# Performance work log

Hardware: AMD Instinct MI355X
Metric: run time of the kernel (lower is better)

## Reference

```python
import jax, jax.numpy as jnp
import numpy as np

ML, KS, L = 3, 7, 7  # mL, kernelSize, L = 2*mL+1


def _conv(img, kern, pad, groups=1):
    # img: [N,C,H,W], kern: [O, C//groups, kh, kw]
    return jax.lax.conv_general_dilated(
        img, kern, (1, 1), [(pad, pad), (pad, pad)],
        dimension_numbers=("NCHW", "OIHW", "NCHW"),
        feature_group_count=groups)


def setup_inputs() -> dict:
    key = jax.random.key(0)
    ks = jax.random.split(key, 16)
    B, MU = 64, 256
    lin = lambda k, fi, fo: (jax.random.normal(k, (fi, fo), jnp.float32) / np.sqrt(fi)).astype(jnp.float32)
    return {
        "x": jax.random.normal(ks[0], (B, 1, MU, MU), jnp.float32),
        "f": jax.random.normal(ks[1], (B, 1, MU, MU), jnp.float32),
        "kernelA": jax.random.normal(ks[2], (B, 1, 3, 3), jnp.float32),
        "fc1_w1": lin(ks[3], 9, 200), "fc1_b1": jnp.zeros((200,), jnp.float32),
        "fc1_w2": lin(ks[4], 200, ML * KS * KS), "fc1_b2": jnp.zeros((ML * KS * KS,), jnp.float32),
        "fc2_w1": lin(ks[5], 9, 200), "fc2_b1": jnp.zeros((200,), jnp.float32),
        "fc2_w2": lin(ks[6], 200, ML * ML * KS * KS), "fc2_b2": jnp.zeros((ML * ML * KS * KS,), jnp.float32),
    }


def reference(x, f, kernelA, fc1_w1, fc1_b1, fc1_w2, fc1_b2, fc2_w1, fc2_b1, fc2_w2, fc2_b2):
    B, _, mu, _ = x.shape
    pad = KS // 2

    # residual r = f - A x   (per-sample 3x3 stencil conv, grouped)
    r = f - jax.vmap(lambda xi, ki: _conv(xi[None], ki[None], 1)[0])(x, kernelA)  # [B,1,mu,mu]

    # meta-MLPs produce per-sample dynamic conv kernels from the 3x3 stencil
    kA = kernelA.reshape(B, 9)
    h1 = jax.nn.relu(kA @ fc1_w1 + fc1_b1)
    w1 = (h1 @ fc1_w2 + fc1_b2).reshape(B, ML, 1, KS, KS)
    h2 = jax.nn.relu(kA @ fc2_w1 + fc2_b1)
    w2 = (h2 @ fc2_w2 + fc2_b2).reshape(B, ML, ML, KS, KS)

    # per-sample dynamic convs (batched via vmap)
    G1 = jax.vmap(lambda ri, wi: _conv(ri[None], wi, pad)[0])(r, w1)    # [B,mL,mu,mu]
    G2 = jax.vmap(lambda gi, wi: _conv(gi[None], wi, pad)[0])(G1, w2)   # [B,mL,mu,mu]
    G = jnp.concatenate([r, G1, G2], axis=1)                            # [B,L,mu,mu]

    # S = A G : apply per-sample stencil to each of the L channels (depthwise)
    S = jax.vmap(lambda gi, ki: _conv(gi[None], jnp.broadcast_to(ki[None], (L, 1, 3, 3)), 1, groups=L)[0])(G, kernelA)
    S = S.reshape(B, L, mu * mu)
    Gf = G.reshape(B, L, mu * mu)
    lr = r.reshape(B, mu * mu, 1)

    # normal equations: (S S^T) K = S r, tiny [L,L] solve per sample
    M = jnp.einsum("bln,bmn->blm", S, S)    # [B,L,L]
    b = jnp.matmul(S, lr)                   # [B,L,1]
    K = jnp.linalg.solve(M, b)              # [B,L,1]

    x_new = x + jnp.matmul(K.transpose(0, 2, 1), Gf).reshape(B, 1, mu, mu)
    return x_new
```

## Files before the change

kernel.cpp:

```cpp
#include <hip/hip_runtime.h>
#include <hip/hip_fp16.h>

#define MU 256
#define NPIX (MU*MU)
#define ML 3
#define KS 7
#define LCH 7
#define NENT 35
#define RBLK 128

typedef _Float16 half2r __attribute__((ext_vector_type(2)));

__device__ __forceinline__ float dot2f(half2r a, half2r b, float c) {
#if __has_builtin(__builtin_amdgcn_fdot2)
    return __builtin_amdgcn_fdot2(a, b, c, false);
#else
    return c + (float)a.x*(float)b.x + (float)a.y*(float)b.y;
#endif
}

__device__ __forceinline__ float4 load_h4(const __half* p) {
    __half2 a = *(const __half2*)p;
    __half2 b = *(const __half2*)(p + 2);
    float2 fa = __half22float2(a), fb = __half22float2(b);
    return make_float4(fa.x, fa.y, fb.x, fb.y);
}

__global__ void mlp_kernel(const float* __restrict__ kernelA,
                           const float* __restrict__ fc1_w1, const float* __restrict__ fc1_b1,
                           const float* __restrict__ fc1_w2, const float* __restrict__ fc1_b2,
                           const float* __restrict__ fc2_w1, const float* __restrict__ fc2_b1,
                           const float* __restrict__ fc2_w2, const float* __restrict__ fc2_b2,
                           half2r* __restrict__ w1p, half2r* __restrict__ w2p) {
    int b = blockIdx.x;
    int t = threadIdx.x;
    __shared__ float kA[9];
    __shared__ float h1[200], h2[200];
    __shared__ float w1s[147];
    __shared__ float w2s[441];
    if (t < 9) kA[t] = kernelA[b*9 + t];
    __syncthreads();
    if (t < 200) {
        float s1 = fc1_b1[t], s2 = fc2_b1[t];
        #pragma unroll
        for (int i = 0; i < 9; ++i) {
            s1 += kA[i] * fc1_w1[i*200 + t];
            s2 += kA[i] * fc2_w1[i*200 + t];
        }
        h1[t] = fmaxf(s1, 0.f);
        h2[t] = fmaxf(s2, 0.f);
    }
    __syncthreads();
    if (t < 147) {
        float s = fc1_b2[t];
        for (int i = 0; i < 200; ++i) s += h1[i] * fc1_w2[i*147 + t];
        w1s[t] = s;
    }
    for (int o = t; o < 441; o += 256) {
        float s = fc2_b2[o];
        for (int i = 0; i < 200; ++i) s += h2[i] * fc2_w2[i*441 + o];
        w2s[o] = s;
    }
    __syncthreads();
    for (int u = t; u < 168; u += 256) {
        int grp = u / 8, p = u % 8;
        int co = grp % 3, i = grp / 3;
        const float* w = &w1s[co*49 + i*7];
        float lo, hi;
        if (p < 4) { lo = (p == 0) ? 0.f : w[2*p - 1]; hi = w[2*p]; }
        else       { int q = p - 4; lo = w[2*q]; hi = (q == 3) ? 0.f : w[2*q + 1]; }
        half2r hp; hp.x = (_Float16)lo; hp.y = (_Float16)hi;
        w1p[(size_t)b*168 + u] = hp;
    }
    for (int u = t; u < 504; u += 256) {
        int grp = u / 8, p = u % 8;
        int co = grp % 3, i = (grp / 3) % 7, c = grp / 21;
        const float* w = &w2s[co*147 + c*49 + i*7];
        float lo, hi;
        if (p < 4) { lo = (p == 0) ? 0.f : w[2*p - 1]; hi = w[2*p]; }
        else       { int q = p - 4; lo = w[2*q]; hi = (q == 3) ? 0.f : w[2*q + 1]; }
        half2r hp; hp.x = (_Float16)lo; hp.y = (_Float16)hi;
        w2p[(size_t)b*504 + u] = hp;
    }
}

__global__ __launch_bounds__(256) void res_g1_kernel(
        const float* __restrict__ x, const float* __restrict__ f,
        const float* __restrict__ kA, const half2r* __restrict__ w1p,
        __half* __restrict__ r, __half* __restrict__ G1) {
    int b = blockIdx.z;
    __shared__ float xt[24][144];
    __shared__ _Float16 rt[22][136];
    int tx = threadIdx.x;
    int ty = threadIdx.y;
    int tid = ty*64 + tx;
    int x0 = blockIdx.x*128, y0 = blockIdx.y*16;
    const float* xb = x + (size_t)b*NPIX;
    const float* fb = f + (size_t)b*NPIX;
    const half2r* wp = w1p + (size_t)b*168;
    float k[9];
    #pragma unroll
    for (int i = 0; i < 9; ++i) k[i] = kA[b*9 + i];

    for (int u = tid; u < 24*36; u += 256) {
        int row = u / 36, q4 = u % 36;
        int yy = y0 + row - 4;
        int xx = x0 - 8 + q4*4;
        float4 vv = make_float4(0.f, 0.f, 0.f, 0.f);
        if (yy >= 0 && yy < MU && xx >= 0 && xx < MU)
            vv = *(const float4*)(xb + yy*MU + xx);
        *(float4*)&xt[row][q4*4] = vv;
    }
    __syncthreads();

    for (int u = tid; u < 22*34; u += 256) {
        int row = u / 34, c4 = u % 34;
        int Y = y0 - 3 + row;
        int X = x0 - 4 + 4*c4;
        bool inb = (Y >= 0 && Y < MU && X >= 0 && X < MU);
        float4 fv = make_float4(0.f, 0.f, 0.f, 0.f);
        if (inb) fv = *(const float4*)(fb + Y*MU + X);
        float fr[4] = {fv.x, fv.y, fv.z, fv.w};
        float rr[4];
        #pragma unroll
        for (int cc = 0; cc < 4; ++cc) {
            float s = 0.f;
            #pragma unroll
            for (int di = 0; di < 3; ++di)
                #pragma unroll
                for (int dj = 0; dj < 3; ++dj)
                    s += xt[row + di][4*c4 + 3 + cc + dj] * k[di*3 + dj];
            rr[cc] = inb ? (fr[cc] - s) : 0.f;
        }
        __half2 h01 = __float22half2_rn(make_float2(rr[0], rr[1]));
        __half2 h23 = __float22half2_rn(make_float2(rr[2], rr[3]));
        *(__half2*)&rt[row][4*c4]     = h01;
        *(__half2*)&rt[row][4*c4 + 2] = h23;
    }
    __syncthreads();

    float accA[3][4], accB[3][4];
    #pragma unroll
    for (int co = 0; co < 3; ++co)
        #pragma unroll
        for (int dy = 0; dy < 4; ++dy) { accA[co][dy] = 0.f; accB[co][dy] = 0.f; }

    int ry = ty*4;
    #pragma unroll
    for (int ir = 0; ir < 10; ++ir) {
        half2r P[5];
        #pragma unroll
        for (int q = 0; q < 5; ++q)
            P[q] = *(const half2r*)&rt[ry + ir][2*tx + 2*q];
        #pragma unroll
        for (int dy = 0; dy < 4; ++dy) {
            int i = ir - dy;
            if (i >= 0 && i <= 6) {
                #pragma unroll
                for (int co = 0; co < 3; ++co) {
                    const half2r* wv = wp + (i*3 + co)*8;
                    accA[co][dy] = dot2f(P[0], wv[0], accA[co][dy]);
                    accA[co][dy] = dot2f(P[1], wv[1], accA[co][dy]);
                    accA[co][dy] = dot2f(P[2], wv[2], accA[co][dy]);
                    accA[co][dy] = dot2f(P[3], wv[3], accA[co][dy]);
                    accB[co][dy] = dot2f(P[1], wv[4], accB[co][dy]);
                    accB[co][dy] = dot2f(P[2], wv[5], accB[co][dy]);
                    accB[co][dy] = dot2f(P[3], wv[6], accB[co][dy]);
                    accB[co][dy] = dot2f(P[4], wv[7], accB[co][dy]);
                }
            }
        }
    }
    #pragma unroll
    for (int dy = 0; dy < 4; ++dy) {
        size_t pr = (size_t)b*NPIX + (size_t)(y0 + ry + dy)*MU + x0 + 2*tx;
        *(__half2*)&r[pr] = *(__half2*)&rt[3 + ry + dy][4 + 2*tx];
        size_t p = (size_t)b*3*NPIX + (size_t)(y0 + ry + dy)*MU + x0 + 2*tx;
        #pragma unroll
        for (int co = 0; co < 3; ++co)
            *(__half2*)&G1[p + (size_t)co*NPIX] =
                __float22half2_rn(make_float2(accA[co][dy], accB[co][dy]));
    }
}

__global__ __launch_bounds__(256) void conv7_g2(
        const __half* __restrict__ G1, const half2r* __restrict__ w2p,
        __half* __restrict__ G2) {
    int b = blockIdx.z;
    __shared__ _Float16 tile[3][14][136];
    int tx = threadIdx.x;
    int ty = threadIdx.y;
    int tid = ty*64 + tx;
    int x0 = blockIdx.x*128, y0 = blockIdx.y*8;
    const __half* g1b = G1 + (size_t)b*3*NPIX;
    const half2r* wp = w2p + (size_t)b*504;

    for (int u = tid; u < 3*14*34; u += 256) {
        int c = u / (14*34);
        int rem = u % (14*34);
        int row = rem / 34, q4 = rem % 34;
        int yy = y0 + row - 3;
        int xx = x0 - 4 + q4*4;
        ushort4 vv = make_ushort4(0, 0, 0, 0);
        if (yy >= 0 && yy < MU && xx >= 0 && xx < MU)
            vv = *(const ushort4*)(g1b + (size_t)c*NPIX + yy*MU + xx);
        *(ushort4*)&tile[c][row][q4*4] = vv;
    }
    __syncthreads();

    float accA[3][2], accB[3][2];
    #pragma unroll
    for (int co = 0; co < 3; ++co)
        #pragma unroll
        for (int dy = 0; dy < 2; ++dy) { accA[co][dy] = 0.f; accB[co][dy] = 0.f; }

    int ry = ty*2;
    #pragma unroll
    for (int c = 0; c < 3; ++c) {
        #pragma unroll
        for (int ir = 0; ir < 8; ++ir) {
            half2r P[5];
            #pragma unroll
            for (int q = 0; q < 5; ++q)
                P[q] = *(const half2r*)&tile[c][ry + ir][2*tx + 2*q];
            #pragma unroll
            for (int dy = 0; dy < 2; ++dy) {
                int i = ir - dy;
                if (i >= 0 && i <= 6) {
                    #pragma unroll
                    for (int co = 0; co < 3; ++co) {
                        const half2r* wv = wp + ((c*7 + i)*3 + co)*8;
                        accA[co][dy] = dot2f(P[0], wv[0], accA[co][dy]);
                        accA[co][dy] = dot2f(P[1], wv[1], accA[co][dy]);
                        accA[co][dy] = dot2f(P[2], wv[2], accA[co][dy]);
                        accA[co][dy] = dot2f(P[3], wv[3], accA[co][dy]);
                        accB[co][dy] = dot2f(P[1], wv[4], accB[co][dy]);
                        accB[co][dy] = dot2f(P[2], wv[5], accB[co][dy]);
                        accB[co][dy] = dot2f(P[3], wv[6], accB[co][dy]);
                        accB[co][dy] = dot2f(P[4], wv[7], accB[co][dy]);
                    }
                }
            }
        }
    }
    #pragma unroll
    for (int dy = 0; dy < 2; ++dy) {
        size_t p = (size_t)b*3*NPIX + (size_t)(y0 + ry + dy)*MU + x0 + 2*tx;
        #pragma unroll
        for (int co = 0; co < 3; ++co)
            *(__half2*)&G2[p + (size_t)co*NPIX] =
                __float22half2_rn(make_float2(accA[co][dy], accB[co][dy]));
    }
}

__global__ __launch_bounds__(256, 4) void reduce_kernel(
        const __half* __restrict__ r, const __half* __restrict__ G1,
        const __half* __restrict__ G2, const float* __restrict__ kA,
        float* __restrict__ partial) {
    int b = blockIdx.z;
    __shared__ float tile[7][10][72];
    __shared__ float wsum[NENT][4];
    int tx = threadIdx.x;
    int ty = threadIdx.y;
    int tid = ty*64 + tx;
    float k[9];
    #pragma unroll
    for (int i = 0; i < 9; ++i) k[i] = kA[b*9 + i];

    const __half* srcs[7] = {
        r  + (size_t)b*NPIX,
        G1 + (size_t)b*3*NPIX, G1 + (size_t)b*3*NPIX + NPIX, G1 + (size_t)b*3*NPIX + 2*NPIX,
        G2 + (size_t)b*3*NPIX, G2 + (size_t)b*3*NPIX + NPIX, G2 + (size_t)b*3*NPIX + 2*NPIX
    };

    int x0 = blockIdx.x*64;
    int ysub = blockIdx.y*8;

    #pragma unroll
    for (int c = 0; c < 7; ++c) {
        const __half* src = srcs[c];
        for (int u = tid; u < 10*18; u += 256) {
            int row = u / 18, q4 = u % 18;
            int yy = ysub + row - 1;
            int xx = x0 - 4 + q4*4;
            float4 vv = make_float4(0.f, 0.f, 0.f, 0.f);
            if (yy >= 0 && yy < MU && xx >= 0 && xx < MU)
                vv = load_h4(src + yy*MU + xx);
            *(float4*)&tile[c][row][q4*4] = vv;
        }
    }
    __syncthreads();

    float acc[64];
    #pragma unroll
    for (int e = 0; e < 64; ++e) acc[e] = 0.f;

    int ry = ty*2;
    float S_all[7][2];
    #pragma unroll
    for (int c = 0; c < 7; ++c) {
        float S0 = 0.f, S1 = 0.f;
        #pragma unroll
        for (int t = 0; t < 4; ++t) {
            float v0 = tile[c][ry + t][tx + 3];
            float v1 = tile[c][ry + t][tx + 4];
            float v2 = tile[c][ry + t][tx + 5];
            float e0 = v0*k[0] + v1*k[1] + v2*k[2];
            float e1 = v0*k[3] + v1*k[4] + v2*k[5];
            float e2 = v0*k[6] + v1*k[7] + v2*k[8];
            if (t == 0) { S0 += e0; }
            if (t == 1) { S0 += e1; S1 += e0; }
            if (t == 2) { S0 += e2; S1 += e1; }
            if (t == 3) {           S1 += e2; }
        }
        S_all[c][0] = S0; S_all[c][1] = S1;
    }
    #pragma unroll
    for (int dy = 0; dy < 2; ++dy) {
        float rv = tile[0][ry + dy + 1][tx + 4];
        int idx = 0;
        #pragma unroll
        for (int l = 0; l < 7; ++l) {
            #pragma unroll
            for (int m = l; m < 7; ++m) {
                acc[idx] += S_all[l][dy] * S_all[m][dy];
                ++idx;
            }
        }
        #pragma unroll
        for (int l = 0; l < 7; ++l) acc[28 + l] += S_all[l][dy] * rv;
    }

    #pragma unroll
    for (int step = 0; step < 6; ++step) {
        const int mask = 1 << step;
        const int nh = 32 >> step;
        bool hi = (tx & mask) != 0;
        #pragma unroll
        for (int i = 0; i < nh; ++i) {
            float send = hi ? acc[i] : acc[i + nh];
            float got = __shfl_xor(send, mask);
            acc[i] = (hi ? acc[i + nh] : acc[i]) + got;
        }
    }
    int ent = ((tx&1)<<5) | ((tx&2)<<3) | ((tx&4)<<1)
            | ((tx&8)>>1) | ((tx&16)>>3) | ((tx&32)>>5);
    if (ent < NENT) wsum[ent][ty] = acc[0];
    __syncthreads();
    if (tid < NENT) {
        float s = wsum[tid][0] + wsum[tid][1] + wsum[tid][2] + wsum[tid][3];
        int blockLinear = blockIdx.y*4 + blockIdx.x;
        partial[((size_t)b*NENT + tid)*RBLK + blockLinear] = s;
    }
}

__global__ void reduce2_kernel(const float* __restrict__ partial,
                               double* __restrict__ M, double* __restrict__ bv) {
    int b = blockIdx.x;
    int wave = threadIdx.x >> 6;
    int lane = threadIdx.x & 63;
    for (int e = wave; e < NENT; e += 4) {
        const float* p = partial + ((size_t)b*NENT + e)*RBLK;
        double s = (double)p[lane] + (double)p[lane + 64];
        #pragma unroll
        for (int off = 32; off; off >>= 1) s += __shfl_down(s, off);
        if (lane == 0) {
            if (e < 28) M[b*28 + e] = s;
            else        bv[b*7 + (e - 28)] = s;
        }
    }
}

__global__ __launch_bounds__(64, 1) void solve_kernel(
        const double* __restrict__ M, const double* __restrict__ bv,
        float* __restrict__ K, int B) {
    int b = blockIdx.x*64 + threadIdx.x;
    if (b >= B) return;
    double A[7][8];
    int idx = 0;
    #pragma unroll
    for (int l = 0; l < 7; ++l)
        #pragma unroll
        for (int m = l; m < 7; ++m) {
            double v = M[b*28 + idx];
            A[l][m] = v;
            A[m][l] = v;
            ++idx;
        }
    #pragma unroll
    for (int l = 0; l < 7; ++l) A[l][7] = bv[b*7 + l];

    #pragma unroll
    for (int col = 0; col < 7; ++col) {
        int piv = col;
        double mx = fabs(A[col][col]);
        #pragma unroll
        for (int rr = 0; rr < 7; ++rr) {
            if (rr > col) {
                double a = fabs(A[rr][col]);
                if (a > mx) { mx = a; piv = rr; }
            }
        }
        #pragma unroll
        for (int rr = 0; rr < 7; ++rr) {
            if (rr > col) {
                bool c = (rr == piv);
                #pragma unroll
                for (int cc = 0; cc < 8; ++cc) {
                    double t0 = A[col][cc], t1 = A[rr][cc];
                    A[col][cc] = c ? t1 : t0;
                    A[rr][cc]  = c ? t0 : t1;
                }
            }
        }
        double d = A[col][col];
        #pragma unroll
        for (int rr = 0; rr < 7; ++rr) {
            if (rr > col) {
                double fct = A[rr][col] / d;
                #pragma unroll
                for (int cc = 0; cc < 8; ++cc) A[rr][cc] -= fct * A[col][cc];
            }
        }
    }
    double Kv[7];
    #pragma unroll
    for (int rr = 6; rr >= 0; --rr) {
        double s = A[rr][7];
        #pragma unroll
        for (int cc = 0; cc < 7; ++cc)
            if (cc > rr) s -= A[rr][cc] * Kv[cc];
        Kv[rr] = s / A[rr][rr];
    }
    #pragma unroll
    for (int l = 0; l < 7; ++l) K[b*7 + l] = (float)Kv[l];
}

__global__ void update_kernel(const float* __restrict__ x, const __half* __restrict__ r,
                              const __half* __restrict__ G1, const __half* __restrict__ G2,
                              const float* __restrict__ K, float* __restrict__ out) {
    int b = blockIdx.z;
    int p4 = blockIdx.x*256 + threadIdx.x;
    float k0 = K[b*7+0], k1 = K[b*7+1], k2 = K[b*7+2], k3 = K[b*7+3];
    float k4 = K[b*7+4], k5 = K[b*7+5], k6 = K[b*7+6];
    size_t q  = (size_t)b*(NPIX/4) + p4;
    size_t e0 = ((size_t)b*3*NPIX) + (size_t)p4*4;
    size_t er = ((size_t)b*NPIX) + (size_t)p4*4;

    float4 xv = ((const float4*)x)[q];
    float4 rv = load_h4(r + er);
    float4 a  = load_h4(G1 + e0);
    float4 bb = load_h4(G1 + e0 + NPIX);
    float4 c  = load_h4(G1 + e0 + 2*(size_t)NPIX);
    float4 d  = load_h4(G2 + e0);
    float4 e  = load_h4(G2 + e0 + NPIX);
    float4 g  = load_h4(G2 + e0 + 2*(size_t)NPIX);
    float4 o;
    o.x = xv.x + k0*rv.x + k1*a.x + k2*bb.x + k3*c.x + k4*d.x + k5*e.x + k6*g.x;
    o.y = xv.y + k0*rv.y + k1*a.y + k2*bb.y + k3*c.y + k4*d.y + k5*e.y + k6*g.y;
    o.z = xv.z + k0*rv.z + k1*a.z + k2*bb.z + k3*c.z + k4*d.z + k5*e.z + k6*g.z;
    o.w = xv.w + k0*rv.w + k1*a.w + k2*bb.w + k3*c.w + k4*d.w + k5*e.w + k6*g.w;
    ((float4*)out)[q] = o;
}

extern "C" void kernel_launch(void* const* d_in, const int* in_sizes, int n_in,
                              void* d_out, int out_size, void* d_ws, size_t ws_size,
                              hipStream_t stream) {
    const float* x       = (const float*)d_in[0];
    const float* f       = (const float*)d_in[1];
    const float* kernelA = (const float*)d_in[2];
    const float* fc1_w1  = (const float*)d_in[3];
    const float* fc1_b1  = (const float*)d_in[4];
    const float* fc1_w2  = (const float*)d_in[5];
    const float* fc1_b2  = (const float*)d_in[6];
    const float* fc2_w1  = (const float*)d_in[7];
    const float* fc2_b1  = (const float*)d_in[8];
    const float* fc2_w2  = (const float*)d_in[9];
    const float* fc2_b2  = (const float*)d_in[10];
    float* out = (float*)d_out;

    const int B = in_sizes[2] / 9;

    double*  Mws = (double*)d_ws;
    double*  bws = Mws + (size_t)B*28;
    float*   Kv  = (float*)(bws + (size_t)B*7);
    float*   partial = Kv + (size_t)B*7;
    half2r*  w1p = (half2r*)(partial + (size_t)B*NENT*RBLK);
    half2r*  w2p = w1p + (size_t)B*168;
    __half*  r   = (__half*)(w2p + (size_t)B*504);
    __half*  G1  = r  + (size_t)B*NPIX;
    __half*  G2  = G1 + (size_t)B*3*NPIX;

    dim3 cblk(64, 4);
    dim3 rgrd(MU/64, MU/8, B);
    dim3 g1grd(MU/128, MU/16, B);
    dim3 g2grd(MU/128, MU/8, B);

    hipLaunchKernelGGL(mlp_kernel, dim3(B), dim3(256), 0, stream,
                       kernelA, fc1_w1, fc1_b1, fc1_w2, fc1_b2,
                       fc2_w1, fc2_b1, fc2_w2, fc2_b2, w1p, w2p);
    hipLaunchKernelGGL(res_g1_kernel, g1grd, cblk, 0, stream, x, f, kernelA, w1p, r, G1);
    hipLaunchKernelGGL(conv7_g2, g2grd, cblk, 0, stream, G1, w2p, G2);
    hipLaunchKernelGGL(reduce_kernel, rgrd, cblk, 0, stream, r, G1, G2, kernelA, partial);
    hipLaunchKernelGGL(reduce2_kernel, dim3(B), dim3(256), 0, stream, partial, Mws, bws);
    hipLaunchKernelGGL(solve_kernel, dim3((B + 63)/64), dim3(64), 0, stream, Mws, bws, Kv, B);
    hipLaunchKernelGGL(update_kernel, dim3(NPIX/1024, 1, B), dim3(256), 0, stream,
                       x, r, G1, G2, Kv, out);
}
```

Baseline: 165.8 us.

## Double-buffer reduce kernel channel tiles to overlap global loads with stencil compute

The reduce kernel no longer stages all 7 channel tiles in shared memory at once. It keeps two 10x72 buffers and prefetches the next channel's halo into registers while computing the current channel's stencil. This cuts LDS use from about 20KB to about 6KB per block, which may allow higher occupancy, and it overlaps global latency with compute. The cost is seven block-wide barriers in place of one, and each thread now issues at most one load per channel.

```diff
diff --git a/kernel.cpp b/kernel.cpp
--- a/kernel.cpp
+++ b/kernel.cpp
@@ -22,6 +22,13 @@
 __device__ __forceinline__ float4 load_h4(const __half* p) {
     __half2 a = *(const __half2*)p;
     __half2 b = *(const __half2*)(p + 2);
+    float2 fa = __half22float2(a), fb = __half22float2(b);
+    return make_float4(fa.x, fa.y, fb.x, fb.y);
+}
+
+__device__ __forceinline__ float4 h4_to_f4(ushort4 u) {
+    __half2 a = *(__half2*)&u.x;
+    __half2 b = *(__half2*)&u.z;
     float2 fa = __half22float2(a), fb = __half22float2(b);
     return make_float4(fa.x, fa.y, fb.x, fb.y);
 }
@@ -258,7 +265,7 @@
         const __half* __restrict__ G2, const float* __restrict__ kA,
         float* __restrict__ partial) {
     int b = blockIdx.z;
-    __shared__ float tile[7][10][72];
+    __shared__ float buf[2][10][72];
     __shared__ float wsum[NENT][4];
     int tx = threadIdx.x;
     int ty = threadIdx.y;
@@ -276,35 +283,35 @@
     int x0 = blockIdx.x*64;
     int ysub = blockIdx.y*8;
 
-    #pragma unroll
-    for (int c = 0; c < 7; ++c) {
-        const __half* src = srcs[c];
-        for (int u = tid; u < 10*18; u += 256) {
-            int row = u / 18, q4 = u % 18;
-            int yy = ysub + row - 1;
-            int xx = x0 - 4 + q4*4;
-            float4 vv = make_float4(0.f, 0.f, 0.f, 0.f);
-            if (yy >= 0 && yy < MU && xx >= 0 && xx < MU)
-                vv = load_h4(src + yy*MU + xx);
-            *(float4*)&tile[c][row][q4*4] = vv;
-        }
-    }
-    __syncthreads();
-
-    float acc[64];
-    #pragma unroll
-    for (int e = 0; e < 64; ++e) acc[e] = 0.f;
+    int srow = tid / 18, sq4 = tid % 18;
+    bool sact = tid < 180;
+    int syy = ysub + srow - 1;
+    int sxx = x0 - 4 + sq4*4;
+    bool sinb = sact && syy >= 0 && syy < MU && sxx >= 0 && sxx < MU;
+    size_t soff = (size_t)syy*MU + sxx;
+
+    {
+        ushort4 pre = make_ushort4(0, 0, 0, 0);
+        if (sinb) pre = *(const ushort4*)(srcs[0] + soff);
+        if (sact) *(float4*)&buf[0][srow][sq4*4] = h4_to_f4(pre);
+    }
+    __syncthreads();
 
     int ry = ty*2;
     float S_all[7][2];
+    float rv[2];
+
     #pragma unroll
     for (int c = 0; c < 7; ++c) {
+        ushort4 nxt = make_ushort4(0, 0, 0, 0);
+        if (c < 6 && sinb) nxt = *(const ushort4*)(srcs[c + 1] + soff);
+
         float S0 = 0.f, S1 = 0.f;
         #pragma unroll
         for (int t = 0; t < 4; ++t) {
-            float v0 = tile[c][ry + t][tx + 3];
-            float v1 = tile[c][ry + t][tx + 4];
-            float v2 = tile[c][ry + t][tx + 5];
+            float v0 = buf[c & 1][ry + t][tx + 3];
+            float v1 = buf[c & 1][ry + t][tx + 4];
+            float v2 = buf[c & 1][ry + t][tx + 5];
             float e0 = v0*k[0] + v1*k[1] + v2*k[2];
             float e1 = v0*k[3] + v1*k[4] + v2*k[5];
             float e2 = v0*k[6] + v1*k[7] + v2*k[8];
@@ -314,10 +321,22 @@
             if (t == 3) {           S1 += e2; }
         }
         S_all[c][0] = S0; S_all[c][1] = S1;
-    }
+        if (c == 0) {
+            rv[0] = buf[0][ry + 1][tx + 4];
+            rv[1] = buf[0][ry + 2][tx + 4];
+        }
+
+        if (c < 6 && sact)
+            *(float4*)&buf[(c + 1) & 1][srow][sq4*4] = h4_to_f4(nxt);
+        __syncthreads();
+    }
+
+    float acc[64];
+    #pragma unroll
+    for (int e = 0; e < 64; ++e) acc[e] = 0.f;
+
     #pragma unroll
     for (int dy = 0; dy < 2; ++dy) {
-        float rv = tile[0][ry + dy + 1][tx + 4];
         int idx = 0;
         #pragma unroll
         for (int l = 0; l < 7; ++l) {
@@ -328,7 +347,7 @@
             }
         }
         #pragma unroll
-        for (int l = 0; l < 7; ++l) acc[28 + l] += S_all[l][dy] * rv;
+        for (int l = 0; l < 7; ++l) acc[28 + l] += S_all[l][dy] * rv[dy];
     }
 
     #pragma unroll
```

Measured after the change: 166.5 us. No clear change (+0.4%).
